# Optimization experiments

Hardware: AMD Instinct MI355X
Metric: run time of the kernel (lower is better)

Reference implementation:

```python
import jax, jax.numpy as jnp
import numpy as np

INIT_TAU = 2.0     # init_tau
V_TH = 1.0         # v_threshold
V_RESET = 0.0      # v_reset
SG_SLOPE = 10.0    # fast-sigmoid surrogate slope
IN_SZ = 8192
OUT_SZ = 8192


def setup_inputs() -> dict:
    key = jax.random.key(0)
    k1, k2, k3, k4 = jax.random.split(key, 4)
    x = jax.random.normal(k1, (IN_SZ,), jnp.float32)
    u = jax.random.normal(k2, (OUT_SZ,), jnp.float32)
    # eligibility trace dL-free state, same shape as the dense kernel
    J_u_W = jax.random.normal(k3, (IN_SZ, OUT_SZ), jnp.float32) * 0.01
    W = jax.random.normal(k4, (IN_SZ, OUT_SZ), jnp.float32) * (1.0 / np.sqrt(IN_SZ))
    return {"x": x, "u": u, "J_u_W": J_u_W, "W": W}


def reference(x, u, J_u_W, W):
    """One OSTL step (the f_fwd path: cell update + eligibility-trace update).

    Cell (SpikingBlockMod with dense connection + LIF dynamics):
      I      = x @ W
      u_new  = sigmoid(init_tau) * u + I
      s      = H(u_new - v_th)               (heaviside spike)
      u_out  = u_new - stop_grad(s) * (v_th - v_reset)   (detached soft reset)

    Trace update (per-parameter, here only the kernel W):
      grad_u_u = sig_tau (diagonal), grad_u_W = x[:, None]
      J_u_W'   = sig_tau * J_u_W + x[:, None]
    """
    sig_tau = jax.nn.sigmoid(jnp.asarray(INIT_TAU, x.dtype))
    I = x @ W                                  # [out]
    u_new = sig_tau * u + I                    # [out]
    v = u_new - V_TH
    s = (v > 0).astype(x.dtype)                # [out] spikes
    u_out = u_new - s * (V_TH - V_RESET)       # detached reset
    J_u_W_new = sig_tau * J_u_W + x[:, None]   # [in, out] eligibility trace
    return (u_out, J_u_W_new, s)
```

## Files before the change

### kernel.cpp

```cpp
#include <hip/hip_runtime.h>

#define IN_SZ 8192
#define OUT_SZ 8192

#define SIG_TAU 0.8807970779778823f

#define GEMV_ROWS   64
#define GEMV_CHUNKS (IN_SZ / GEMV_ROWS)
#define GEMV_TILES  (OUT_SZ / 1024)
#define GEMV_BLOCKS (GEMV_CHUNKS * GEMV_TILES)
#define JUP_BLOCKS  IN_SZ

typedef float v4f __attribute__((ext_vector_type(4)));

__global__ __launch_bounds__(256) void main_kernel(
        const float* __restrict__ x,
        const float* __restrict__ J,
        const float* __restrict__ W,
        float* __restrict__ Jout,
        float* __restrict__ partial) {
    const int bid = blockIdx.x;
    const int tid = threadIdx.x;

    if (bid < GEMV_BLOCKS) {
        __shared__ float xs[GEMV_ROWS];
        const int tile  = bid & (GEMV_TILES - 1);
        const int chunk = bid / GEMV_TILES;
        const int col0  = tile * 1024 + tid * 4;
        const int row0  = chunk * GEMV_ROWS;

        if (tid < GEMV_ROWS) xs[tid] = x[row0 + tid];
        __syncthreads();

        float4 acc = make_float4(0.f, 0.f, 0.f, 0.f);
        const float* wp = W + (size_t)row0 * OUT_SZ + col0;
#pragma unroll 8
        for (int r = 0; r < GEMV_ROWS; ++r) {
            float4 w = *(const float4*)wp;
            float xi = xs[r];
            acc.x += xi * w.x;
            acc.y += xi * w.y;
            acc.z += xi * w.z;
            acc.w += xi * w.w;
            wp += OUT_SZ;
        }
        *(float4*)(partial + (size_t)chunk * OUT_SZ + col0) = acc;
    } else {
        const int row = bid - GEMV_BLOCKS;
        const float xi = x[row];
        const v4f* jp = (const v4f*)(J + (size_t)row * OUT_SZ);
        v4f* op = (v4f*)(Jout + (size_t)row * OUT_SZ);
#pragma unroll
        for (int c = 0; c < OUT_SZ / 4 / 256; ++c) {
            v4f v = __builtin_nontemporal_load(&jp[c * 256 + tid]);
            v.x = SIG_TAU * v.x + xi;
            v.y = SIG_TAU * v.y + xi;
            v.z = SIG_TAU * v.z + xi;
            v.w = SIG_TAU * v.w + xi;
            __builtin_nontemporal_store(v, &op[c * 256 + tid]);
        }
    }
}

__global__ __launch_bounds__(256) void finalize_reduce_kernel(
        const float* __restrict__ u,
        const float* __restrict__ partial,
        float* __restrict__ out) {
    const int j = blockIdx.x * blockDim.x + threadIdx.x;
    if (j >= OUT_SZ) return;
    float a0 = 0.f, a1 = 0.f, a2 = 0.f, a3 = 0.f;
#pragma unroll 4
    for (int c = 0; c < GEMV_CHUNKS; c += 4) {
        a0 += partial[(size_t)(c + 0) * OUT_SZ + j];
        a1 += partial[(size_t)(c + 1) * OUT_SZ + j];
        a2 += partial[(size_t)(c + 2) * OUT_SZ + j];
        a3 += partial[(size_t)(c + 3) * OUT_SZ + j];
    }
    float I     = (a0 + a1) + (a2 + a3);
    float u_new = SIG_TAU * u[j] + I;
    float s     = (u_new - 1.0f > 0.0f) ? 1.0f : 0.0f;
    out[j] = u_new - s;
    out[(size_t)OUT_SZ + (size_t)IN_SZ * OUT_SZ + j] = s;
}

__global__ void zeroI_kernel(float* __restrict__ I) {
    int j = blockIdx.x * blockDim.x + threadIdx.x;
    if (j < OUT_SZ) I[j] = 0.0f;
}

template <int ROWS>
__global__ void gemv_partial_atomic_kernel(const float* __restrict__ x,
                                           const float* __restrict__ W,
                                           float* __restrict__ Iacc) {
    __shared__ float xs[ROWS];
    const int tid  = threadIdx.x;
    const int col0 = blockIdx.x * 1024 + tid * 4;
    const int row0 = blockIdx.y * ROWS;

    if (tid < ROWS) xs[tid] = x[row0 + tid];
    __syncthreads();

    float4 acc = make_float4(0.f, 0.f, 0.f, 0.f);
    const float* wp = W + (size_t)row0 * OUT_SZ + col0;
#pragma unroll 8
    for (int r = 0; r < ROWS; ++r) {
        float4 w = *(const float4*)wp;
        float xi = xs[r];
        acc.x += xi * w.x;
        acc.y += xi * w.y;
        acc.z += xi * w.z;
        acc.w += xi * w.w;
        wp += OUT_SZ;
    }
    atomicAdd(&Iacc[col0 + 0], acc.x);
    atomicAdd(&Iacc[col0 + 1], acc.y);
    atomicAdd(&Iacc[col0 + 2], acc.z);
    atomicAdd(&Iacc[col0 + 3], acc.w);
}

__global__ void finalize_kernel(const float* __restrict__ u,
                                float* __restrict__ out) {
    int j = blockIdx.x * blockDim.x + threadIdx.x;
    if (j >= OUT_SZ) return;
    float I     = out[j];
    float u_new = SIG_TAU * u[j] + I;
    float s     = (u_new - 1.0f > 0.0f) ? 1.0f : 0.0f;
    out[j] = u_new - s;
    out[(size_t)OUT_SZ + (size_t)IN_SZ * OUT_SZ + j] = s;
}

__global__ void jup_kernel(const float* __restrict__ x,
                           const float* __restrict__ J,
                           float* __restrict__ Jout) {
    const int row = blockIdx.x;
    const float xi = x[row];
    const float4* jp = (const float4*)(J + (size_t)row * OUT_SZ);
    float4* op = (float4*)(Jout + (size_t)row * OUT_SZ);
    const int tid = threadIdx.x;
#pragma unroll
    for (int c = 0; c < OUT_SZ / 4 / 256; ++c) {
        float4 v = jp[c * 256 + tid];
        v.x = SIG_TAU * v.x + xi;
        v.y = SIG_TAU * v.y + xi;
        v.z = SIG_TAU * v.z + xi;
        v.w = SIG_TAU * v.w + xi;
        op[c * 256 + tid] = v;
    }
}

extern "C" void kernel_launch(void* const* d_in, const int* in_sizes, int n_in,
                              void* d_out, int out_size, void* d_ws, size_t ws_size,
                              hipStream_t stream) {
    const float* x = (const float*)d_in[0];
    const float* u = (const float*)d_in[1];
    const float* J = (const float*)d_in[2];
    const float* W = (const float*)d_in[3];
    float* out = (float*)d_out;

    const size_t ws_needed = (size_t)GEMV_CHUNKS * OUT_SZ * sizeof(float);

    if (d_ws != nullptr && ws_size >= ws_needed) {
        float* partial = (float*)d_ws;
        main_kernel<<<GEMV_BLOCKS + JUP_BLOCKS, 256, 0, stream>>>(
            x, J, W, out + OUT_SZ, partial);
        finalize_reduce_kernel<<<(OUT_SZ + 255) / 256, 256, 0, stream>>>(
            u, partial, out);
    } else {
        jup_kernel<<<IN_SZ, 256, 0, stream>>>(x, J, out + OUT_SZ);
        zeroI_kernel<<<(OUT_SZ + 255) / 256, 256, 0, stream>>>(out);
        gemv_partial_atomic_kernel<64><<<dim3(OUT_SZ / 1024, IN_SZ / 64), 256, 0, stream>>>(x, W, out);
        finalize_kernel<<<(OUT_SZ + 255) / 256, 256, 0, stream>>>(u, out);
    }
}
```

Measured before the change: 629.6 us.

## Split fused kernel into J-update halves with mixed nontemporal and cached access

Measured after the change: 613.2 us. 1.03x faster.

```diff
diff --git a/kernel.cpp b/kernel.cpp
--- a/kernel.cpp
+++ b/kernel.cpp
@@ -9,57 +9,67 @@
 #define GEMV_CHUNKS (IN_SZ / GEMV_ROWS)
 #define GEMV_TILES  (OUT_SZ / 1024)
 #define GEMV_BLOCKS (GEMV_CHUNKS * GEMV_TILES)
-#define JUP_BLOCKS  IN_SZ
 
 typedef float v4f __attribute__((ext_vector_type(4)));
 
-__global__ __launch_bounds__(256) void main_kernel(
+template <bool NT>
+__global__ __launch_bounds__(256) void jup_half_kernel(
         const float* __restrict__ x,
         const float* __restrict__ J,
+        float* __restrict__ Jout,
+        int row0) {
+    const int row = row0 + blockIdx.x;
+    const int tid = threadIdx.x;
+    const float xi = x[row];
+    const v4f* jp = (const v4f*)(J + (size_t)row * OUT_SZ);
+    v4f* op = (v4f*)(Jout + (size_t)row * OUT_SZ);
+
+    v4f v[8];
+#pragma unroll
+    for (int c = 0; c < 8; ++c) {
+        if (NT) v[c] = __builtin_nontemporal_load(&jp[c * 256 + tid]);
+        else    v[c] = jp[c * 256 + tid];
+    }
+#pragma unroll
+    for (int c = 0; c < 8; ++c) {
+        v4f r;
+        r.x = SIG_TAU * v[c].x + xi;
+        r.y = SIG_TAU * v[c].y + xi;
+        r.z = SIG_TAU * v[c].z + xi;
+        r.w = SIG_TAU * v[c].w + xi;
+        if (NT) __builtin_nontemporal_store(r, &op[c * 256 + tid]);
+        else    op[c * 256 + tid] = r;
+    }
+}
+
+__global__ __launch_bounds__(256) void gemv_partial_kernel(
+        const float* __restrict__ x,
         const float* __restrict__ W,
-        float* __restrict__ Jout,
         float* __restrict__ partial) {
-    const int bid = blockIdx.x;
-    const int tid = threadIdx.x;
+    __shared__ float xs[GEMV_ROWS];
+    const int bid   = blockIdx.x;
+    const int tid   = threadIdx.x;
+    const int tile  = bid & (GEMV_TILES - 1);
+    const int chunk = bid / GEMV_TILES;
+    const int col0  = tile * 1024 + tid * 4;
+    const int row0  = chunk * GEMV_ROWS;
 
-    if (bid < GEMV_BLOCKS) {
-        __shared__ float xs[GEMV_ROWS];
-        const int tile  = bid & (GEMV_TILES - 1);
-        const int chunk = bid / GEMV_TILES;
-        const int col0  = tile * 1024 + tid * 4;
-        const int row0  = chunk * GEMV_ROWS;
+    if (tid < GEMV_ROWS) xs[tid] = x[row0 + tid];
+    __syncthreads();
 
-        if (tid < GEMV_ROWS) xs[tid] = x[row0 + tid];
-        __syncthreads();
-
-        float4 acc = make_float4(0.f, 0.f, 0.f, 0.f);
-        const float* wp = W + (size_t)row0 * OUT_SZ + col0;
+    float4 acc = make_float4(0.f, 0.f, 0.f, 0.f);
+    const float* wp = W + (size_t)row0 * OUT_SZ + col0;
 #pragma unroll 8
-        for (int r = 0; r < GEMV_ROWS; ++r) {
-            float4 w = *(const float4*)wp;
-            float xi = xs[r];
-            acc.x += xi * w.x;
-            acc.y += xi * w.y;
-            acc.z += xi * w.z;
-            acc.w += xi * w.w;
-            wp += OUT_SZ;
-        }
-        *(float4*)(partial + (size_t)chunk * OUT_SZ + col0) = acc;
-    } else {
-        const int row = bid - GEMV_BLOCKS;
-        const float xi = x[row];
-        const v4f* jp = (const v4f*)(J + (size_t)row * OUT_SZ);
-        v4f* op = (v4f*)(Jout + (size_t)row * OUT_SZ);
-#pragma unroll
-        for (int c = 0; c < OUT_SZ / 4 / 256; ++c) {
-            v4f v = __builtin_nontemporal_load(&jp[c * 256 + tid]);
-            v.x = SIG_TAU * v.x + xi;
-            v.y = SIG_TAU * v.y + xi;
-            v.z = SIG_TAU * v.z + xi;
-            v.w = SIG_TAU * v.w + xi;
-            __builtin_nontemporal_store(v, &op[c * 256 + tid]);
-        }
+    for (int r = 0; r < GEMV_ROWS; ++r) {
+        float4 w = *(const float4*)wp;
+        float xi = xs[r];
+        acc.x += xi * w.x;
+        acc.y += xi * w.y;
+        acc.z += xi * w.z;
+        acc.w += xi * w.w;
+        wp += OUT_SZ;
     }
+    *(float4*)(partial + (size_t)chunk * OUT_SZ + col0) = acc;
 }
 
 __global__ __launch_bounds__(256) void finalize_reduce_kernel(
@@ -161,8 +171,12 @@
 
     if (d_ws != nullptr && ws_size >= ws_needed) {
         float* partial = (float*)d_ws;
-        main_kernel<<<GEMV_BLOCKS + JUP_BLOCKS, 256, 0, stream>>>(
-            x, J, W, out + OUT_SZ, partial);
+        float* Jout = out + OUT_SZ;
+
+        jup_half_kernel<true ><<<IN_SZ / 2, 256, 0, stream>>>(x, J, Jout, 0);
+        jup_half_kernel<false><<<IN_SZ / 2, 256, 0, stream>>>(x, J, Jout, IN_SZ / 2);
+
+        gemv_partial_kernel<<<GEMV_BLOCKS, 256, 0, stream>>>(x, W, partial);
         finalize_reduce_kernel<<<(OUT_SZ + 255) / 256, 256, 0, stream>>>(
             u, partial, out);
     } else {
```
